# Performance work log

Measured on AMD Instinct MI355X. Metric: run time of the kernel, lower is better.

Reference implementation:

```python
import jax, jax.numpy as jnp
import numpy as np

T, B, F, H, N = 256, 256, 128, 1024, 2


def setup_inputs() -> dict:
    key = jax.random.key(0)
    ks = jax.random.split(key, 12)
    s_in = 1.0 / np.sqrt(H)  # PyTorch LSTM/Linear init scale ~ U(-1/sqrt(H), 1/sqrt(H))
    u = lambda k, shape: jax.random.uniform(k, shape, jnp.float32, -s_in, s_in)
    inp = {
        "x": jax.random.normal(ks[0], (T, B, F), jnp.float32),
        "W_ih0": u(ks[1], (4 * H, F)),
        "W_hh0": u(ks[2], (4 * H, H)),
        "b_ih0": u(ks[3], (4 * H,)),
        "b_hh0": u(ks[4], (4 * H,)),
        "W_ih1": u(ks[5], (4 * H, H)),
        "W_hh1": u(ks[6], (4 * H, H)),
        "b_ih1": u(ks[7], (4 * H,)),
        "b_hh1": u(ks[8], (4 * H,)),
        "W_lin": u(ks[9], (F, H)),
        "b_lin": u(ks[10], (F,)),
        "bs": B,
    }
    return inp


def _lstm_layer(x, W_ih, W_hh, b_ih, b_hh):
    # x: (T, B, in), returns out (T, B, H), (h_T, c_T) each (B, H)
    # Precompute input projections for all timesteps in one big GEMM.
    xW = jnp.einsum('tbf,gf->tbg', x, W_ih) + b_ih + b_hh  # (T, B, 4H)
    h0 = jnp.zeros((x.shape[1], W_hh.shape[1]), x.dtype)

    def step(carry, xw_t):
        h, c = carry
        gates = xw_t + h @ W_hh.T  # (B, 4H); PyTorch gate order i, f, g, o
        i, f, g, o = jnp.split(gates, 4, axis=-1)
        c = jax.nn.sigmoid(f) * c + jax.nn.sigmoid(i) * jnp.tanh(g)
        h = jax.nn.sigmoid(o) * jnp.tanh(c)
        return (h, c), h

    (h_T, c_T), out = jax.lax.scan(step, (h0, h0), xW)
    return out, h_T, c_T


def reference(x, W_ih0, W_hh0, b_ih0, b_hh0, W_ih1, W_hh1, b_ih1, b_hh1, W_lin, b_lin, bs):
    # Stacked 2-layer LSTM with zero initial state (self.h is None on fresh call).
    out0, h0_T, c0_T = _lstm_layer(x, W_ih0, W_hh0, b_ih0, b_hh0)
    out1, h1_T, c1_T = _lstm_layer(out0, W_ih1, W_hh1, b_ih1, b_hh1)
    # Original: y = linear(out[0]) -> first timestep of top layer output.
    y = out1[0] @ W_lin.T + b_lin  # (B, F)
    h_n = jnp.stack([h0_T, h1_T])  # (N, B, H)
    c_n = jnp.stack([c0_T, c1_T])  # (N, B, H)
    return y, h_n, c_n
```

## Files before the change

### kernel.cpp

```cpp
#include <hip/hip_runtime.h>
#include <stdint.h>


typedef __bf16 bf16x8 __attribute__((ext_vector_type(8)));
typedef float  f32x4  __attribute__((ext_vector_type(4)));
typedef unsigned short ushort8v __attribute__((ext_vector_type(8)));
typedef unsigned short ushort4v __attribute__((ext_vector_type(4)));
typedef unsigned short ushort2v __attribute__((ext_vector_type(2)));
typedef unsigned int   uint4v   __attribute__((ext_vector_type(4)));
typedef __attribute__((address_space(1))) unsigned int as1_u32;
typedef __attribute__((address_space(3))) unsigned int as3_u32;

#define T_STEPS 256
#define BATCH   256
#define HDIM    1024
#define GDIM    4096
#define FDIM    128
#define AS_STRIDE 2080

static __device__ __forceinline__ float bf2f(unsigned short u) {
  union { unsigned int i; float f; } v; v.i = ((unsigned int)u) << 16; return v.f;
}
static __device__ __forceinline__ unsigned short f2bf(float f) {
  return __builtin_bit_cast(unsigned short, (__bf16)f);
}
static __device__ __forceinline__ float sigm(float x) { return 1.f / (1.f + __expf(-x)); }
static __device__ __forceinline__ float tanh_f(float x) { return 2.f / (1.f + __expf(-2.f * x)) - 1.f; }

static __device__ __forceinline__ void vl1_inv() {
  asm volatile("buffer_inv" ::: "memory");
}

__global__ void conv_bf16(const float* __restrict__ s, unsigned short* __restrict__ d, int n) {
  int i = blockIdx.x * 256 + threadIdx.x;
  if (i < n) d[i] = f2bf(s[i]);
}

__global__ void diag_kernel(float* out, int n, float v) {
  int i = blockIdx.x * 256 + threadIdx.x;
  if (i < n) out[i] = v;
}

__device__ __forceinline__ void post_stamp(unsigned int* st, unsigned int gen, bool fast) {
  if (!fast) __builtin_amdgcn_fence(__ATOMIC_RELEASE, "agent");
  __hip_atomic_store(st, gen, __ATOMIC_RELAXED, __HIP_MEMORY_SCOPE_AGENT);
}

__device__ __forceinline__ void poll_all(unsigned int* stamps, unsigned int target) {
  unsigned int* p = stamps + (threadIdx.x & 31) * 32;
  for (unsigned int it = 0; it < (1u << 15); ++it) {
    unsigned int gv = __hip_atomic_load(p, __ATOMIC_RELAXED, __HIP_MEMORY_SCOPE_AGENT);
    if (__all((int)(gv - target) >= 0)) return;
    if (it > 16) __builtin_amdgcn_s_sleep(1);
  }
}

__device__ __forceinline__ void stage64(const unsigned short* __restrict__ hsrc,
                                        char* AsB, int r0, int wv, int lane) {
  #pragma unroll
  for (int p = 0; p < 8; ++p) {
    int idx = p * 8 + wv;
    int row = idx >> 1, half = idx & 1;
    const char* gsrc = (const char*)(hsrc + (size_t)(r0 + row) * HDIM + half * 512) + lane * 16;
    char* ldst = AsB + row * AS_STRIDE + half * 1024;
    __builtin_amdgcn_global_load_lds((const as1_u32*)gsrc, (as3_u32*)ldst, 16, 0, 0);
  }
}

__global__ __launch_bounds__(256) void gemm_bt_xw(
    const unsigned short* __restrict__ A,
    const unsigned short* __restrict__ B,
    unsigned short* __restrict__ xw,
    int K)
{
  const int tid = threadIdx.x, lane = tid & 63, w = tid >> 6;
  const int m0 = blockIdx.x * 128;
  const int n0 = blockIdx.y * 128;
  __shared__ unsigned short As[128 * 64];
  __shared__ unsigned short Bs[128 * 64];
  const int mrow0 = (w & 1) * 64, ncol0 = (w >> 1) * 64;
  const int quad = lane >> 4;

  f32x4 acc[4][4];
  #pragma unroll
  for (int i = 0; i < 4; ++i)
    #pragma unroll
    for (int j = 0; j < 4; ++j) acc[i][j] = f32x4{0.f, 0.f, 0.f, 0.f};

  const int kiter = K >> 6;
  for (int ki = 0; ki < kiter; ++ki) {
    const int k0 = ki * 64;
    __syncthreads();
    #pragma unroll
    for (int i = 0; i < 4; ++i) {
      int obase = (w * 4 + i) * 1024;
      int o = obase + lane * 16;
      int row = o >> 7; int kb = o & 127;
      const char* ga = (const char*)A + ((size_t)(m0 + row) * K + k0) * 2 + kb;
      const char* gb = (const char*)B + ((size_t)(n0 + row) * K + k0) * 2 + kb;
      __builtin_amdgcn_global_load_lds((const as1_u32*)ga, (as3_u32*)((char*)As + obase), 16, 0, 0);
      __builtin_amdgcn_global_load_lds((const as1_u32*)gb, (as3_u32*)((char*)Bs + obase), 16, 0, 0);
    }
    __syncthreads();
    #pragma unroll
    for (int kk = 0; kk < 2; ++kk) {
      bf16x8 af[4], bfr[4];
      #pragma unroll
      for (int mt = 0; mt < 4; ++mt)
        af[mt] = *(const bf16x8*)(As + (mrow0 + mt * 16 + (lane & 15)) * 64 + kk * 32 + quad * 8);
      #pragma unroll
      for (int nt = 0; nt < 4; ++nt)
        bfr[nt] = *(const bf16x8*)(Bs + (ncol0 + nt * 16 + (lane & 15)) * 64 + kk * 32 + quad * 8);
      #pragma unroll
      for (int mt = 0; mt < 4; ++mt)
        #pragma unroll
        for (int nt = 0; nt < 4; ++nt)
          acc[mt][nt] = __builtin_amdgcn_mfma_f32_16x16x32_bf16(af[mt], bfr[nt], acc[mt][nt], 0, 0, 0);
    }
  }
  #pragma unroll
  for (int mt = 0; mt < 4; ++mt) {
    int m = m0 + mrow0 + mt * 16 + quad * 4;
    int tl = m >> 8, b = m & 255;
    #pragma unroll
    for (int nt = 0; nt < 4; ++nt) {
      int col = n0 + ncol0 + nt * 16 + (lane & 15);
      ushort4v v;
      v.x = f2bf(acc[mt][nt][0]); v.y = f2bf(acc[mt][nt][1]);
      v.z = f2bf(acc[mt][nt][2]); v.w = f2bf(acc[mt][nt][3]);
      *(ushort4v*)(xw + ((size_t)tl * GDIM + col) * BATCH + b) = v;
    }
  }
}

__device__ __forceinline__ bool probe_chk(unsigned int* probeBuf, unsigned int* stamps,
                                          unsigned int salt, unsigned int target,
                                          unsigned int* flagLds) {
  const int wg = blockIdx.x, mi = wg & 7, ni = wg >> 3;
  const int tid = threadIdx.x;
  if (tid == 0) probeBuf[wg * 32] = salt ^ (unsigned int)wg;
  __syncthreads();
  if (tid == 0)
    __hip_atomic_store(stamps + ni * 32, target, __ATOMIC_RELAXED, __HIP_MEMORY_SCOPE_AGENT);
  poll_all(stamps, target);
  vl1_inv();
  if (tid == 0) {
    unsigned int bad = 0;
    for (int k = 0; k < 32; ++k) {
      int member = mi + 8 * k;
      unsigned int v = probeBuf[member * 32];
      if (v != (salt ^ (unsigned int)member)) bad = 1;
    }
    *flagLds = bad;
  }
  __syncthreads();
  return (*flagLds == 0);
}

__global__ __launch_bounds__(512, 2) void lstm_layer0_kernel(
    const unsigned short* __restrict__ xbf,
    const float* __restrict__ Wih,
    const float* __restrict__ Whh,
    const float* __restrict__ bih,
    const float* __restrict__ bhh,
    unsigned short* __restrict__ slab,
    unsigned short* __restrict__ hx,
    float* __restrict__ cstate,
    int t0, int ch_len, unsigned int gen_base,
    float* __restrict__ dout_h,
    float* __restrict__ dout_c,
    unsigned int* __restrict__ bar,
    unsigned int* __restrict__ probe)
{
  const int tid = threadIdx.x, lane = tid & 63, wv = tid >> 6;
  const int quad = lane >> 4, l15 = lane & 15;
  const int g = wv & 3, kh = wv >> 2;
  const int wg = blockIdx.x;
  const int mi = wg & 7, ni = wg >> 3;
  const int r0 = mi * 32, hc0 = ni * 32;
  unsigned int* stamps = bar + mi * 1024;

  __shared__ unsigned short As[32 * (AS_STRIDE / 2)];
  __shared__ float gbuf[8][32][36];
  __shared__ unsigned int flagLds;

  bf16x8 whh[2][16];
  #pragma unroll
  for (int nt = 0; nt < 2; ++nt) {
    const float* wrow = Whh + (size_t)(g * HDIM + hc0 + nt * 16 + l15) * HDIM + kh * 512 + quad * 8;
    #pragma unroll
    for (int kk = 0; kk < 16; ++kk) {
      f32x4 f0 = *(const f32x4*)(wrow + kk * 32);
      f32x4 f1 = *(const f32x4*)(wrow + kk * 32 + 4);
      bf16x8 r;
      r[0] = (__bf16)f0[0]; r[1] = (__bf16)f0[1]; r[2] = (__bf16)f0[2]; r[3] = (__bf16)f0[3];
      r[4] = (__bf16)f1[0]; r[5] = (__bf16)f1[1]; r[6] = (__bf16)f1[2]; r[7] = (__bf16)f1[3];
      whh[nt][kk] = r;
    }
  }
  bf16x8 wih[2][2];
  #pragma unroll
  for (int nt = 0; nt < 2; ++nt) {
    const float* wrow = Wih + (size_t)(g * HDIM + hc0 + nt * 16 + l15) * FDIM + kh * 64 + quad * 8;
    #pragma unroll
    for (int kk = 0; kk < 2; ++kk) {
      f32x4 f0 = *(const f32x4*)(wrow + kk * 32);
      f32x4 f1 = *(const f32x4*)(wrow + kk * 32 + 4);
      bf16x8 r;
      r[0] = (__bf16)f0[0]; r[1] = (__bf16)f0[1]; r[2] = (__bf16)f0[2]; r[3] = (__bf16)f0[3];
      r[4] = (__bf16)f1[0]; r[5] = (__bf16)f1[1]; r[6] = (__bf16)f1[2]; r[7] = (__bf16)f1[3];
      wih[nt][kk] = r;
    }
  }

  const int hcl = tid & 31, rg2 = tid >> 5;
  float bias[4];
  #pragma unroll
  for (int b4 = 0; b4 < 4; ++b4)
    bias[b4] = bih[b4 * HDIM + hc0 + hcl] + bhh[b4 * HDIM + hc0 + hcl];

  float c[2];
  #pragma unroll
  for (int r = 0; r < 2; ++r)
    c[r] = (t0 == 0) ? 0.f : cstate[(size_t)(r0 + rg2 * 2 + r) * HDIM + hc0 + hcl];

  unsigned int salt = 0x9E3779B9u ^ (gen_base * 2654435761u);
  bool fast = probe_chk(probe, stamps, salt, gen_base + 1u, &flagLds);

  const int tend = t0 + ch_len;

  if (t0 > 0)
    stage64(hx + (size_t)((t0 - 1) & 1) * (BATCH * HDIM), (char*)As, r0, wv, lane);

  f32x4 acc[2][2];
  #pragma unroll
  for (int mt = 0; mt < 2; ++mt)
    #pragma unroll
    for (int nt = 0; nt < 2; ++nt) acc[mt][nt] = f32x4{0.f, 0.f, 0.f, 0.f};
  #pragma unroll
  for (int j = 0; j < 2; ++j) {
    bf16x8 af[2];
    #pragma unroll
    for (int mt = 0; mt < 2; ++mt)
      af[mt] = *(const bf16x8*)(xbf + (size_t)(t0 * BATCH + r0 + mt * 16 + l15) * FDIM + kh * 64 + j * 32 + quad * 8);
    #pragma unroll
    for (int mt = 0; mt < 2; ++mt)
      #pragma unroll
      for (int nt = 0; nt < 2; ++nt)
        acc[mt][nt] = __builtin_amdgcn_mfma_f32_16x16x32_bf16(af[mt], wih[nt][j], acc[mt][nt], 0, 0, 0);
  }
  __syncthreads();

  #pragma unroll 1
  for (int t = t0; t < tend; ++t) {
    if (t > 0) {
      #pragma unroll
      for (int j = 0; j < 16; ++j) {
        bf16x8 af[2];
        #pragma unroll
        for (int mt = 0; mt < 2; ++mt)
          af[mt] = *(const bf16x8*)((const char*)As + (mt * 16 + l15) * AS_STRIDE + (kh * 16 + j) * 64 + quad * 16);
        #pragma unroll
        for (int mt = 0; mt < 2; ++mt)
          #pragma unroll
          for (int nt = 0; nt < 2; ++nt)
            acc[mt][nt] = __builtin_amdgcn_mfma_f32_16x16x32_bf16(af[mt], whh[nt][j], acc[mt][nt], 0, 0, 0);
      }
    }

    #pragma unroll
    for (int mt = 0; mt < 2; ++mt)
      #pragma unroll
      for (int nt = 0; nt < 2; ++nt) {
        int hl = nt * 16 + l15;
        int rq = mt * 16 + quad * 4;
        *(f32x4*)&gbuf[wv][hl][rq] = acc[mt][nt];
      }
    __syncthreads();

    unsigned short* hdst = slab + (size_t)(t - t0 + 1) * (BATCH * HDIM);
    unsigned short* hxd  = hx + (size_t)(t & 1) * (BATCH * HDIM);
    #pragma unroll
    for (int r = 0; r < 2; ++r) {
      int row = rg2 * 2 + r;
      float gi = gbuf[0][hcl][row] + gbuf[4][hcl][row] + bias[0];
      float gf = gbuf[1][hcl][row] + gbuf[5][hcl][row] + bias[1];
      float gg = gbuf[2][hcl][row] + gbuf[6][hcl][row] + bias[2];
      float go = gbuf[3][hcl][row] + gbuf[7][hcl][row] + bias[3];
      float iv = sigm(gi), fv = sigm(gf), gv = tanh_f(gg), ov = sigm(go);
      float cn = fv * c[r] + iv * gv;
      c[r] = cn;
      float hv = ov * tanh_f(cn);
      int gidx = (r0 + row) * HDIM + hc0 + hcl;
      unsigned short hb = f2bf(hv);
      hxd[gidx] = hb;
      hdst[gidx] = hb;
      if (t == tend - 1) cstate[gidx] = cn;
      if (t == T_STEPS - 1) { dout_h[gidx] = hv; dout_c[gidx] = cn; }
    }
    __syncthreads();

    if (t != tend - 1) {
      const unsigned int tgt = gen_base + 2u + (unsigned int)(t - t0);
      if (tid == 0) post_stamp(stamps + ni * 32, tgt, fast);

      #pragma unroll
      for (int mt = 0; mt < 2; ++mt)
        #pragma unroll
        for (int nt = 0; nt < 2; ++nt) acc[mt][nt] = f32x4{0.f, 0.f, 0.f, 0.f};
      #pragma unroll
      for (int j = 0; j < 2; ++j) {
        bf16x8 af[2];
        #pragma unroll
        for (int mt = 0; mt < 2; ++mt)
          af[mt] = *(const bf16x8*)(xbf + (size_t)((t + 1) * BATCH + r0 + mt * 16 + l15) * FDIM + kh * 64 + j * 32 + quad * 8);
        #pragma unroll
        for (int mt = 0; mt < 2; ++mt)
          #pragma unroll
          for (int nt = 0; nt < 2; ++nt)
            acc[mt][nt] = __builtin_amdgcn_mfma_f32_16x16x32_bf16(af[mt], wih[nt][j], acc[mt][nt], 0, 0, 0);
      }

      poll_all(stamps, tgt);
      if (fast) vl1_inv();
      else __builtin_amdgcn_fence(__ATOMIC_ACQUIRE, "agent");
      stage64(hx + (size_t)(t & 1) * (BATCH * HDIM), (char*)As, r0, wv, lane);
      __syncthreads();
    }
  }
}

__global__ __launch_bounds__(512, 2) void lstm_layer1_kernel(
    const unsigned short* __restrict__ xw,
    const float* __restrict__ Whh,
    const float* __restrict__ bih,
    const float* __restrict__ bhh,
    unsigned short* __restrict__ hpp,
    float* __restrict__ cstate,
    int t0, int ch_len, unsigned int gen_base,
    unsigned short* __restrict__ h1t0,
    float* __restrict__ dout_h,
    float* __restrict__ dout_c,
    unsigned int* __restrict__ bar,
    unsigned int* __restrict__ probe)
{
  const int tid = threadIdx.x, lane = tid & 63, wv = tid >> 6;
  const int quad = lane >> 4, l15 = lane & 15;
  const int g = wv & 3, kh = wv >> 2;
  const int wg = blockIdx.x;
  const int mi = wg & 7, ni = wg >> 3;
  const int r0 = mi * 32, hc0 = ni * 32;
  unsigned int* stamps = bar + mi * 1024;

  __shared__ unsigned short As[32 * (AS_STRIDE / 2)];
  __shared__ float gbuf[8][32][36];
  __shared__ unsigned int flagLds;

  bf16x8 whh[2][16];
  #pragma unroll
  for (int nt = 0; nt < 2; ++nt) {
    const float* wrow = Whh + (size_t)(g * HDIM + hc0 + nt * 16 + l15) * HDIM + kh * 512 + quad * 8;
    #pragma unroll
    for (int kk = 0; kk < 16; ++kk) {
      f32x4 f0 = *(const f32x4*)(wrow + kk * 32);
      f32x4 f1 = *(const f32x4*)(wrow + kk * 32 + 4);
      bf16x8 r;
      r[0] = (__bf16)f0[0]; r[1] = (__bf16)f0[1]; r[2] = (__bf16)f0[2]; r[3] = (__bf16)f0[3];
      r[4] = (__bf16)f1[0]; r[5] = (__bf16)f1[1]; r[6] = (__bf16)f1[2]; r[7] = (__bf16)f1[3];
      whh[nt][kk] = r;
    }
  }

  const int hcl = tid & 31, rg2 = tid >> 5;
  float bias[4];
  #pragma unroll
  for (int b4 = 0; b4 < 4; ++b4)
    bias[b4] = bih[b4 * HDIM + hc0 + hcl] + bhh[b4 * HDIM + hc0 + hcl];

  float c[2];
  #pragma unroll
  for (int r = 0; r < 2; ++r)
    c[r] = (t0 == 0) ? 0.f : cstate[(size_t)(r0 + rg2 * 2 + r) * HDIM + hc0 + hcl];

  unsigned int salt = 0xB5297A4Du ^ (gen_base * 2654435761u);
  bool fast = probe_chk(probe, stamps, salt, gen_base + 1u, &flagLds);

  const int tend = t0 + ch_len;

  if (t0 > 0)
    stage64(hpp + (size_t)((t0 - 1) & 1) * (BATCH * HDIM), (char*)As, r0, wv, lane);
  float xwv[4][2];
  #pragma unroll
  for (int g4 = 0; g4 < 4; ++g4) {
    const unsigned short* xp =
        xw + ((size_t)0 * GDIM + g4 * HDIM + hc0 + hcl) * BATCH + r0 + rg2 * 2;
    ushort2v u = *(const ushort2v*)xp;
    xwv[g4][0] = bf2f(u.x); xwv[g4][1] = bf2f(u.y);
  }
  __syncthreads();

  #pragma unroll 1
  for (int t = t0; t < tend; ++t) {
    f32x4 acc[2][2];
    #pragma unroll
    for (int mt = 0; mt < 2; ++mt)
      #pragma unroll
      for (int nt = 0; nt < 2; ++nt) acc[mt][nt] = f32x4{0.f, 0.f, 0.f, 0.f};

    if (t > 0) {
      #pragma unroll
      for (int j = 0; j < 16; ++j) {
        bf16x8 af[2];
        #pragma unroll
        for (int mt = 0; mt < 2; ++mt)
          af[mt] = *(const bf16x8*)((const char*)As + (mt * 16 + l15) * AS_STRIDE + (kh * 16 + j) * 64 + quad * 16);
        #pragma unroll
        for (int mt = 0; mt < 2; ++mt)
          #pragma unroll
          for (int nt = 0; nt < 2; ++nt)
            acc[mt][nt] = __builtin_amdgcn_mfma_f32_16x16x32_bf16(af[mt], whh[nt][j], acc[mt][nt], 0, 0, 0);
      }
    }

    #pragma unroll
    for (int mt = 0; mt < 2; ++mt)
      #pragma unroll
      for (int nt = 0; nt < 2; ++nt) {
        int hl = nt * 16 + l15;
        int rq = mt * 16 + quad * 4;
        *(f32x4*)&gbuf[wv][hl][rq] = acc[mt][nt];
      }
    __syncthreads();

    unsigned short* hdst = hpp + (size_t)(t & 1) * (BATCH * HDIM);
    #pragma unroll
    for (int r = 0; r < 2; ++r) {
      int row = rg2 * 2 + r;
      float gi = gbuf[0][hcl][row] + gbuf[4][hcl][row] + xwv[0][r] + bias[0];
      float gf = gbuf[1][hcl][row] + gbuf[5][hcl][row] + xwv[1][r] + bias[1];
      float gg = gbuf[2][hcl][row] + gbuf[6][hcl][row] + xwv[2][r] + bias[2];
      float go = gbuf[3][hcl][row] + gbuf[7][hcl][row] + xwv[3][r] + bias[3];
      float iv = sigm(gi), fv = sigm(gf), gv = tanh_f(gg), ov = sigm(go);
      float cn = fv * c[r] + iv * gv;
      c[r] = cn;
      float hv = ov * tanh_f(cn);
      int gidx = (r0 + row) * HDIM + hc0 + hcl;
      hdst[gidx] = f2bf(hv);
      if (h1t0 != nullptr && t == 0) h1t0[gidx] = f2bf(hv);
      if (t == tend - 1) cstate[gidx] = cn;
      if (t == T_STEPS - 1) { dout_h[gidx] = hv; dout_c[gidx] = cn; }
    }
    __syncthreads();

    if (t != tend - 1) {
      const unsigned int tgt = gen_base + 2u + (unsigned int)(t - t0);
      if (tid == 0) post_stamp(stamps + ni * 32, tgt, fast);

      #pragma unroll
      for (int g4 = 0; g4 < 4; ++g4) {
        const unsigned short* xp =
            xw + ((size_t)(t + 1 - t0) * GDIM + g4 * HDIM + hc0 + hcl) * BATCH + r0 + rg2 * 2;
        ushort2v u = *(const ushort2v*)xp;
        xwv[g4][0] = bf2f(u.x); xwv[g4][1] = bf2f(u.y);
      }

      poll_all(stamps, tgt);
      if (fast) vl1_inv();
      else __builtin_amdgcn_fence(__ATOMIC_ACQUIRE, "agent");
      stage64(hpp + (size_t)(t & 1) * (BATCH * HDIM), (char*)As, r0, wv, lane);
      __syncthreads();
    }
  }
}

__global__ void y_kernel(const unsigned short* __restrict__ h1t0,
                         const unsigned short* __restrict__ wlin,
                         const float* __restrict__ blin,
                         float* __restrict__ y)
{
  int b = blockIdx.x;
  int f = threadIdx.x;
  const ushort8v* hp = (const ushort8v*)(h1t0 + (size_t)b * HDIM);
  const ushort8v* wp = (const ushort8v*)(wlin + (size_t)f * HDIM);
  float acc = 0.f;
  for (int i = 0; i < HDIM / 8; ++i) {
    ushort8v hv = hp[i], wvv = wp[i];
    #pragma unroll
    for (int j = 0; j < 8; ++j) acc += bf2f(hv[j]) * bf2f(wvv[j]);
  }
  y[b * FDIM + f] = acc + blin[f];
}

extern "C" void kernel_launch(void* const* d_in, const int* in_sizes, int n_in,
                              void* d_out, int out_size, void* d_ws, size_t ws_size,
                              hipStream_t stream) {
  (void)in_sizes; (void)n_in; (void)out_size;
  const float* x    = (const float*)d_in[0];
  const float* Wih0 = (const float*)d_in[1];
  const float* Whh0 = (const float*)d_in[2];
  const float* bih0 = (const float*)d_in[3];
  const float* bhh0 = (const float*)d_in[4];
  const float* Wih1 = (const float*)d_in[5];
  const float* Whh1 = (const float*)d_in[6];
  const float* bih1 = (const float*)d_in[7];
  const float* bhh1 = (const float*)d_in[8];
  const float* Wlin = (const float*)d_in[9];
  const float* blin = (const float*)d_in[10];
  float* out = (float*)d_out;

  const size_t SZ_BAR   = 32768;
  const size_t SZ_PROBE = 32768;
  const size_t SZ_XBF   = (size_t)T_STEPS * BATCH * FDIM * 2;
  const size_t SZ_WIH1  = (size_t)GDIM * HDIM * 2;
  const size_t SZ_WLIN  = (size_t)FDIM * HDIM * 2;
  const size_t SZ_HPP   = (size_t)2 * BATCH * HDIM * 2;
  const size_t SZ_HX    = (size_t)2 * BATCH * HDIM * 2;
  const size_t SZ_H1T0  = (size_t)BATCH * HDIM * 2;
  const size_t SZ_CST   = (size_t)BATCH * HDIM * 4;
  const size_t SLOT     = (size_t)BATCH * HDIM * 2;
  const size_t fixed = SZ_BAR + SZ_PROBE + SZ_XBF + SZ_WIH1 + SZ_WLIN + SZ_HPP + SZ_HX + SZ_H1T0 + 2 * SZ_CST;

  int CH = 0;
  const int cands[5] = {64, 32, 16, 8, 4};
  for (int i = 0; i < 5; ++i) {
    int c = cands[i];
    size_t need = fixed + (size_t)(c + 1) * SLOT + (size_t)c * GDIM * BATCH * 2;
    if (need <= ws_size) { CH = c; break; }
  }
  if (CH == 0) {
    float v = 1.0e6f + (float)(ws_size >> 20);
    diag_kernel<<<(32768 + 255) / 256, 256, 0, stream>>>(out, 32768, v);
    return;
  }

  char* ws = (char*)d_ws;
  size_t o = 0;
  unsigned int*   bar   = (unsigned int*)(ws + o);    o += SZ_BAR;
  unsigned int*   probe = (unsigned int*)(ws + o);    o += SZ_PROBE;
  unsigned short* xbf   = (unsigned short*)(ws + o);  o += SZ_XBF;
  unsigned short* wih1b = (unsigned short*)(ws + o);  o += SZ_WIH1;
  unsigned short* wlinb = (unsigned short*)(ws + o);  o += SZ_WLIN;
  unsigned short* h1pp  = (unsigned short*)(ws + o);  o += SZ_HPP;
  unsigned short* hx0   = (unsigned short*)(ws + o);  o += SZ_HX;
  unsigned short* h1t0  = (unsigned short*)(ws + o);  o += SZ_H1T0;
  float*          c0st  = (float*)(ws + o);           o += SZ_CST;
  float*          c1st  = (float*)(ws + o);           o += SZ_CST;
  unsigned short* slab  = (unsigned short*)(ws + o);  o += (size_t)(CH + 1) * SLOT;
  unsigned short* xw1   = (unsigned short*)(ws + o);  o += (size_t)CH * GDIM * BATCH * 2;

  hipMemsetAsync(bar, 0, SZ_BAR, stream);

  conv_bf16<<<(T_STEPS * BATCH * FDIM + 255) / 256, 256, 0, stream>>>(x, xbf, T_STEPS * BATCH * FDIM);
  conv_bf16<<<(GDIM * HDIM + 255) / 256, 256, 0, stream>>>(Wih1, wih1b, GDIM * HDIM);
  conv_bf16<<<(FDIM * HDIM + 255) / 256, 256, 0, stream>>>(Wlin, wlinb, FDIM * HDIM);

  float* hn0 = out + 32768;
  float* hn1 = out + 32768 + 262144;
  float* cn0 = out + 32768 + 524288;
  float* cn1 = out + 32768 + 524288 + 262144;

  unsigned int gen_base = 0;
  for (int ch = 0; ch < T_STEPS / CH; ++ch) {
    int t0 = ch * CH;
    lstm_layer0_kernel<<<256, 512, 0, stream>>>(
        xbf, Wih0, Whh0, bih0, bhh0, slab, hx0, c0st, t0, CH, gen_base, hn0, cn0, bar, probe);
    gen_base += (unsigned int)CH;
    gemm_bt_xw<<<dim3(CH * 2, 32), 256, 0, stream>>>(
        slab + BATCH * HDIM, wih1b, xw1, HDIM);
    lstm_layer1_kernel<<<256, 512, 0, stream>>>(
        xw1, Whh1, bih1, bhh1, h1pp, c1st, t0, CH, gen_base, h1t0, hn1, cn1, bar, probe);
    gen_base += (unsigned int)CH;
  }

  y_kernel<<<256, 128, 0, stream>>>(h1t0, wlinb, blin, out);
}
```

Baseline: 3.610 ms.

## Replace per-step full barrier with per-chunk producer polling and LDS flags

The recurrent hidden-state buffer is re-laid out so that each producer workgroup's 32 columns form a contiguous chunk. Each wave now polls only the stamps of the producers whose chunks it stages, and copies those chunks into LDS. It then publishes an LDS flag, replacing the block-wide __syncthreads after staging. The MFMA loop is reordered so each wave consumes its own chunks first and spins on the other waves' flags only when it reaches their chunks, with W_hh registers loaded in the matching permuted order. The aim is to overlap cross-workgroup synchronisation with compute instead of waiting for all producers, at the cost of finer-grained spin loops and more complex ordering.

```diff
diff --git a/kernel.cpp b/kernel.cpp
--- a/kernel.cpp
+++ b/kernel.cpp
@@ -7,7 +7,6 @@
 typedef unsigned short ushort8v __attribute__((ext_vector_type(8)));
 typedef unsigned short ushort4v __attribute__((ext_vector_type(4)));
 typedef unsigned short ushort2v __attribute__((ext_vector_type(2)));
-typedef unsigned int   uint4v   __attribute__((ext_vector_type(4)));
 typedef __attribute__((address_space(1))) unsigned int as1_u32;
 typedef __attribute__((address_space(3))) unsigned int as3_u32;
 
@@ -16,7 +15,7 @@
 #define HDIM    1024
 #define GDIM    4096
 #define FDIM    128
-#define AS_STRIDE 2080
+#define HXSLOT  (BATCH * HDIM)
 
 static __device__ __forceinline__ float bf2f(unsigned short u) {
   union { unsigned int i; float f; } v; v.i = ((unsigned int)u) << 16; return v.f;
@@ -55,15 +54,32 @@
   }
 }
 
-__device__ __forceinline__ void stage64(const unsigned short* __restrict__ hsrc,
-                                        char* AsB, int r0, int wv, int lane) {
-  #pragma unroll
-  for (int p = 0; p < 8; ++p) {
-    int idx = p * 8 + wv;
-    int row = idx >> 1, half = idx & 1;
-    const char* gsrc = (const char*)(hsrc + (size_t)(r0 + row) * HDIM + half * 512) + lane * 16;
-    char* ldst = AsB + row * AS_STRIDE + half * 1024;
-    __builtin_amdgcn_global_load_lds((const as1_u32*)gsrc, (as3_u32*)ldst, 16, 0, 0);
+__device__ __forceinline__ void poll_mine(unsigned int* stamps, int g, int kh, unsigned int target) {
+  unsigned int* p = stamps + (kh * 16 + g + 4 * ((int)threadIdx.x & 3)) * 32;
+  for (unsigned int it = 0; it < (1u << 15); ++it) {
+    unsigned int gv = __hip_atomic_load(p, __ATOMIC_RELAXED, __HIP_MEMORY_SCOPE_AGENT);
+    if (__all((int)(gv - target) >= 0)) return;
+    if (it > 16) __builtin_amdgcn_s_sleep(1);
+  }
+}
+
+__device__ __forceinline__ void lds_spin(unsigned int* f, unsigned int need) {
+  for (unsigned int it = 0; it < (1u << 15); ++it) {
+    unsigned int v = __hip_atomic_load(f, __ATOMIC_ACQUIRE, __HIP_MEMORY_SCOPE_WORKGROUP);
+    if ((int)(v - need) >= 0) return;
+    if (it > 8) __builtin_amdgcn_s_sleep(1);
+  }
+}
+
+__device__ __forceinline__ void stage_chunks(const unsigned short* __restrict__ hsrc,
+                                             unsigned short* AsPtr, int r0, int g, int kh, int lane) {
+  #pragma unroll
+  for (int q = 0; q < 4; ++q) {
+    int c = kh * 16 + g + 4 * q;
+    const char* src = (const char*)(hsrc + (size_t)c * 8192 + r0 * 32);
+    char* dst = (char*)AsPtr + c * 2048;
+    __builtin_amdgcn_global_load_lds((const as1_u32*)(src + lane * 16), (as3_u32*)dst, 16, 0, 0);
+    __builtin_amdgcn_global_load_lds((const as1_u32*)(src + 1024 + lane * 16), (as3_u32*)(dst + 1024), 16, 0, 0);
   }
 }
 
@@ -180,22 +196,26 @@
   const int r0 = mi * 32, hc0 = ni * 32;
   unsigned int* stamps = bar + mi * 1024;
 
-  __shared__ unsigned short As[32 * (AS_STRIDE / 2)];
+  __shared__ unsigned short As[32 * 1024];
   __shared__ float gbuf[8][32][36];
+  __shared__ unsigned int cflag[8];
   __shared__ unsigned int flagLds;
 
+  if (tid < 8) cflag[tid] = 0;
+
   bf16x8 whh[2][16];
   #pragma unroll
   for (int nt = 0; nt < 2; ++nt) {
-    const float* wrow = Whh + (size_t)(g * HDIM + hc0 + nt * 16 + l15) * HDIM + kh * 512 + quad * 8;
-    #pragma unroll
-    for (int kk = 0; kk < 16; ++kk) {
-      f32x4 f0 = *(const f32x4*)(wrow + kk * 32);
-      f32x4 f1 = *(const f32x4*)(wrow + kk * 32 + 4);
+    #pragma unroll
+    for (int sl = 0; sl < 16; ++sl) {
+      int jj = ((g + (sl >> 2)) & 3) + 4 * (sl & 3);
+      const float* wrow = Whh + (size_t)(g * HDIM + hc0 + nt * 16 + l15) * HDIM + kh * 512 + jj * 32 + quad * 8;
+      f32x4 f0 = *(const f32x4*)(wrow);
+      f32x4 f1 = *(const f32x4*)(wrow + 4);
       bf16x8 r;
       r[0] = (__bf16)f0[0]; r[1] = (__bf16)f0[1]; r[2] = (__bf16)f0[2]; r[3] = (__bf16)f0[3];
       r[4] = (__bf16)f1[0]; r[5] = (__bf16)f1[1]; r[6] = (__bf16)f1[2]; r[7] = (__bf16)f1[3];
-      whh[nt][kk] = r;
+      whh[nt][sl] = r;
     }
   }
   bf16x8 wih[2][2];
@@ -229,8 +249,12 @@
 
   const int tend = t0 + ch_len;
 
-  if (t0 > 0)
-    stage64(hx + (size_t)((t0 - 1) & 1) * (BATCH * HDIM), (char*)As, r0, wv, lane);
+  if (t0 > 0) {
+    stage_chunks(hx + (size_t)((t0 - 1) & 1) * HXSLOT, As, r0, g, kh, lane);
+    asm volatile("s_waitcnt vmcnt(0)" ::: "memory");
+    if (lane == 0)
+      __hip_atomic_store(&cflag[kh * 4 + g], gen_base + 1u, __ATOMIC_RELEASE, __HIP_MEMORY_SCOPE_WORKGROUP);
+  }
 
   f32x4 acc[2][2];
   #pragma unroll
@@ -249,22 +273,26 @@
       for (int nt = 0; nt < 2; ++nt)
         acc[mt][nt] = __builtin_amdgcn_mfma_f32_16x16x32_bf16(af[mt], wih[nt][j], acc[mt][nt], 0, 0, 0);
   }
-  __syncthreads();
 
   #pragma unroll 1
   for (int t = t0; t < tend; ++t) {
     if (t > 0) {
-      #pragma unroll
-      for (int j = 0; j < 16; ++j) {
+      const unsigned int need = gen_base + 1u + (unsigned int)(t - t0);
+      #pragma unroll
+      for (int sl = 0; sl < 16; ++sl) {
+        const int s = sl >> 2, q = sl & 3;
+        int sg = (g + s) & 3;
+        if (q == 0 && s > 0) lds_spin(&cflag[kh * 4 + sg], need);
+        int cidx = kh * 16 + sg + 4 * q;
         bf16x8 af[2];
         #pragma unroll
         for (int mt = 0; mt < 2; ++mt)
-          af[mt] = *(const bf16x8*)((const char*)As + (mt * 16 + l15) * AS_STRIDE + (kh * 16 + j) * 64 + quad * 16);
+          af[mt] = *(const bf16x8*)((const char*)As + cidx * 2048 + (mt * 16 + l15) * 64 + quad * 16);
         #pragma unroll
         for (int mt = 0; mt < 2; ++mt)
           #pragma unroll
           for (int nt = 0; nt < 2; ++nt)
-            acc[mt][nt] = __builtin_amdgcn_mfma_f32_16x16x32_bf16(af[mt], whh[nt][j], acc[mt][nt], 0, 0, 0);
+            acc[mt][nt] = __builtin_amdgcn_mfma_f32_16x16x32_bf16(af[mt], whh[nt][sl], acc[mt][nt], 0, 0, 0);
       }
     }
 
@@ -279,7 +307,7 @@
     __syncthreads();
 
     unsigned short* hdst = slab + (size_t)(t - t0 + 1) * (BATCH * HDIM);
-    unsigned short* hxd  = hx + (size_t)(t & 1) * (BATCH * HDIM);
+    unsigned short* hxd  = hx + (size_t)(t & 1) * HXSLOT;
     #pragma unroll
     for (int r = 0; r < 2; ++r) {
       int row = rg2 * 2 + r;
@@ -291,9 +319,9 @@
       float cn = fv * c[r] + iv * gv;
       c[r] = cn;
       float hv = ov * tanh_f(cn);
+      unsigned short hb = f2bf(hv);
+      hxd[ni * 8192 + (r0 + row) * 32 + hcl] = hb;
       int gidx = (r0 + row) * HDIM + hc0 + hcl;
-      unsigned short hb = f2bf(hv);
-      hxd[gidx] = hb;
       hdst[gidx] = hb;
       if (t == tend - 1) cstate[gidx] = cn;
       if (t == T_STEPS - 1) { dout_h[gidx] = hv; dout_c[gidx] = cn; }
@@ -321,11 +349,13 @@
             acc[mt][nt] = __builtin_amdgcn_mfma_f32_16x16x32_bf16(af[mt], wih[nt][j], acc[mt][nt], 0, 0, 0);
       }
 
-      poll_all(stamps, tgt);
+      poll_mine(stamps, g, kh, tgt);
       if (fast) vl1_inv();
       else __builtin_amdgcn_fence(__ATOMIC_ACQUIRE, "agent");
-      stage64(hx + (size_t)(t & 1) * (BATCH * HDIM), (char*)As, r0, wv, lane);
-      __syncthreads();
+      stage_chunks(hx + (size_t)(t & 1) * HXSLOT, As, r0, g, kh, lane);
+      asm volatile("s_waitcnt vmcnt(0)" ::: "memory");
+      if (lane == 0)
+        __hip_atomic_store(&cflag[kh * 4 + g], tgt, __ATOMIC_RELEASE, __HIP_MEMORY_SCOPE_WORKGROUP);
     }
   }
 }
@@ -352,22 +382,26 @@
   const int r0 = mi * 32, hc0 = ni * 32;
   unsigned int* stamps = bar + mi * 1024;
 
-  __shared__ unsigned short As[32 * (AS_STRIDE / 2)];
+  __shared__ unsigned short As[32 * 1024];
   __shared__ float gbuf[8][32][36];
+  __shared__ unsigned int cflag[8];
   __shared__ unsigned int flagLds;
 
+  if (tid < 8) cflag[tid] = 0;
+
   bf16x8 whh[2][16];
   #pragma unroll
   for (int nt = 0; nt < 2; ++nt) {
-    const float* wrow = Whh + (size_t)(g * HDIM + hc0 + nt * 16 + l15) * HDIM + kh * 512 + quad * 8;
-    #pragma unroll
-    for (int kk = 0; kk < 16; ++kk) {
-      f32x4 f0 = *(const f32x4*)(wrow + kk * 32);
-      f32x4 f1 = *(const f32x4*)(wrow + kk * 32 + 4);
+    #pragma unroll
+    for (int sl = 0; sl < 16; ++sl) {
+      int jj = ((g + (sl >> 2)) & 3) + 4 * (sl & 3);
+      const float* wrow = Whh + (size_t)(g * HDIM + hc0 + nt * 16 + l15) * HDIM + kh * 512 + jj * 32 + quad * 8;
+      f32x4 f0 = *(const f32x4*)(wrow);
+      f32x4 f1 = *(const f32x4*)(wrow + 4);
       bf16x8 r;
       r[0] = (__bf16)f0[0]; r[1] = (__bf16)f0[1]; r[2] = (__bf16)f0[2]; r[3] = (__bf16)f0[3];
       r[4] = (__bf16)f1[0]; r[5] = (__bf16)f1[1]; r[6] = (__bf16)f1[2]; r[7] = (__bf16)f1[3];
-      whh[nt][kk] = r;
+      whh[nt][sl] = r;
     }
   }
 
@@ -387,8 +421,13 @@
 
   const int tend = t0 + ch_len;
 
-  if (t0 > 0)
-    stage64(hpp + (size_t)((t0 - 1) & 1) * (BATCH * HDIM), (char*)As, r0, wv, lane);
+  if (t0 > 0) {
+    stage_chunks(hpp + (size_t)((t0 - 1) & 1) * HXSLOT, As, r0, g, kh, lane);
+    asm volatile("s_waitcnt vmcnt(0)" ::: "memory");
+    if (lane == 0)
+      __hip_atomic_store(&cflag[kh * 4 + g], gen_base + 1u, __ATOMIC_RELEASE, __HIP_MEMORY_SCOPE_WORKGROUP);
+  }
+
   float xwv[4][2];
   #pragma unroll
   for (int g4 = 0; g4 < 4; ++g4) {
@@ -397,7 +436,6 @@
     ushort2v u = *(const ushort2v*)xp;
     xwv[g4][0] = bf2f(u.x); xwv[g4][1] = bf2f(u.y);
   }
-  __syncthreads();
 
   #pragma unroll 1
   for (int t = t0; t < tend; ++t) {
@@ -408,17 +446,22 @@
       for (int nt = 0; nt < 2; ++nt) acc[mt][nt] = f32x4{0.f, 0.f, 0.f, 0.f};
 
     if (t > 0) {
-      #pragma unroll
-      for (int j = 0; j < 16; ++j) {
+      const unsigned int need = gen_base + 1u + (unsigned int)(t - t0);
+      #pragma unroll
+      for (int sl = 0; sl < 16; ++sl) {
+        const int s = sl >> 2, q = sl & 3;
+        int sg = (g + s) & 3;
+        if (q == 0 && s > 0) lds_spin(&cflag[kh * 4 + sg], need);
+        int cidx = kh * 16 + sg + 4 * q;
         bf16x8 af[2];
         #pragma unroll
         for (int mt = 0; mt < 2; ++mt)
-          af[mt] = *(const bf16x8*)((const char*)As + (mt * 16 + l15) * AS_STRIDE + (kh * 16 + j) * 64 + quad * 16);
+          af[mt] = *(const bf16x8*)((const char*)As + cidx * 2048 + (mt * 16 + l15) * 64 + quad * 16);
         #pragma unroll
         for (int mt = 0; mt < 2; ++mt)
           #pragma unroll
           for (int nt = 0; nt < 2; ++nt)
-            acc[mt][nt] = __builtin_amdgcn_mfma_f32_16x16x32_bf16(af[mt], whh[nt][j], acc[mt][nt], 0, 0, 0);
+            acc[mt][nt] = __builtin_amdgcn_mfma_f32_16x16x32_bf16(af[mt], whh[nt][sl], acc[mt][nt], 0, 0, 0);
       }
     }
 
@@ -432,7 +475,7 @@
       }
     __syncthreads();
 
-    unsigned short* hdst = hpp + (size_t)(t & 1) * (BATCH * HDIM);
+    unsigned short* hxd = hpp + (size_t)(t & 1) * HXSLOT;
     #pragma unroll
     for (int r = 0; r < 2; ++r) {
       int row = rg2 * 2 + r;
@@ -444,9 +487,10 @@
       float cn = fv * c[r] + iv * gv;
       c[r] = cn;
       float hv = ov * tanh_f(cn);
+      unsigned short hb = f2bf(hv);
+      hxd[ni * 8192 + (r0 + row) * 32 + hcl] = hb;
       int gidx = (r0 + row) * HDIM + hc0 + hcl;
-      hdst[gidx] = f2bf(hv);
-      if (h1t0 != nullptr && t == 0) h1t0[gidx] = f2bf(hv);
+      if (h1t0 != nullptr && t == 0) h1t0[gidx] = hb;
       if (t == tend - 1) cstate[gidx] = cn;
       if (t == T_STEPS - 1) { dout_h[gidx] = hv; dout_c[gidx] = cn; }
     }
@@ -464,11 +508,13 @@
         xwv[g4][0] = bf2f(u.x); xwv[g4][1] = bf2f(u.y);
       }
 
-      poll_all(stamps, tgt);
+      poll_mine(stamps, g, kh, tgt);
       if (fast) vl1_inv();
       else __builtin_amdgcn_fence(__ATOMIC_ACQUIRE, "agent");
-      stage64(hpp + (size_t)(t & 1) * (BATCH * HDIM), (char*)As, r0, wv, lane);
-      __syncthreads();
+      stage_chunks(hpp + (size_t)(t & 1) * HXSLOT, As, r0, g, kh, lane);
+      asm volatile("s_waitcnt vmcnt(0)" ::: "memory");
+      if (lane == 0)
+        __hip_atomic_store(&cflag[kh * 4 + g], tgt, __ATOMIC_RELEASE, __HIP_MEMORY_SCOPE_WORKGROUP);
     }
   }
 }
```

New measurement: 3.624 ms. About the same (+0.4%).
